# Performance work log

Measured on AMD Instinct MI355X. Metric: run time of the kernel, lower is better.

## Reference

```python
import jax, jax.numpy as jnp
import numpy as np

B, C, H, W = 2, 256, 360, 360
N1 = N2 = 1024


def setup_inputs() -> dict:
    key = jax.random.key(0)
    ks = jax.random.split(key, 12)
    s = 0.02
    feature = jax.random.normal(ks[0], (B, C, H, W), dtype=jnp.float32)
    # midx rows: [batch_idx, h, w]; frame 0 centers and frame 1 centers
    idx1 = jnp.stack([
        jnp.zeros((N1,), dtype=jnp.int32),
        jax.random.randint(ks[1], (N1,), 0, H, dtype=jnp.int32),
        jax.random.randint(ks[2], (N1,), 0, W, dtype=jnp.int32),
    ])
    idx2 = jnp.stack([
        jnp.ones((N2,), dtype=jnp.int32),
        jax.random.randint(ks[3], (N2,), 0, H, dtype=jnp.int32),
        jax.random.randint(ks[4], (N2,), 0, W, dtype=jnp.int32),
    ])
    w1 = jax.random.normal(ks[5], (256, 256), dtype=jnp.float32) * s
    b1 = jnp.zeros((256,), dtype=jnp.float32)
    w2 = jax.random.normal(ks[6], (256, 128), dtype=jnp.float32) * s
    b2 = jnp.zeros((128,), dtype=jnp.float32)
    w3 = jax.random.normal(ks[7], (128, 32), dtype=jnp.float32) * s
    b3 = jnp.zeros((32,), dtype=jnp.float32)
    w4 = jax.random.normal(ks[8], (32, 1), dtype=jnp.float32) * s
    b4 = jnp.zeros((1,), dtype=jnp.float32)
    return {"feature": feature, "idx1": idx1, "idx2": idx2,
            "w1": w1, "b1": b1, "w2": w2, "b2": b2,
            "w3": w3, "b3": b3, "w4": w4, "b4": b4}


def reference(feature, idx1, idx2, w1, b1, w2, b2, w3, b3, w4, b4):
    # feature: [B,C,H,W] -> [B,H,W,C] (torch .permute(0,2,3,1))
    feat = jnp.transpose(feature, (0, 2, 3, 1))

    def project(midx):
        # irregular gather of per-center features: [N, C]
        x = feat[midx[0], midx[1], midx[2]]
        h = jax.nn.relu(x @ w1 + b1)          # [N, 256]
        return jax.nn.relu(h @ w2 + b2)       # [N, 128]

    f1 = project(idx1)                        # [N1, D]
    f2 = project(idx2)                        # [N2, D]
    # laplacian_dists: broadcast outer difference [N1, N2, D]
    diff = f1[:, None, :] - f2[None, :, :]
    # out_layer = linear_last(D, 32, 1): Linear -> ReLU -> Linear
    h = jax.nn.relu(jnp.einsum('mnd,dk->mnk', diff, w3) + b3)
    out = jnp.einsum('mnk,ko->mno', h, w4) + b4
    return out[..., 0]                        # [N1, N2] similarity
```

## Files before the change

kernel.cpp:

```cpp
#include <hip/hip_runtime.h>

#define NPTS 1024
#define NC 256
#define NH 360
#define NW 360
#define NHW (NH * NW)
#define NCHW (NC * NHW)
#define PPB 8
#define PAD 12

__global__ __launch_bounds__(512) void mlp_kernel(
    const float* __restrict__ feature,
    const int* __restrict__ idx1,
    const int* __restrict__ idx2,
    const float* __restrict__ w1, const float* __restrict__ b1,
    const float* __restrict__ w2, const float* __restrict__ b2,
    const float* __restrict__ w3, const float* __restrict__ b3,
    float* __restrict__ pq)
{
    __shared__ float Xs[256 * PAD];
    __shared__ float H1s[256 * PAD];
    __shared__ float F2s[128 * PAD];

    const int tid = threadIdx.x;
    const int base = blockIdx.x * PPB;

    {
        const int c = tid & 255;
        const int pg = (tid >> 8) * 4;
        float v[4];
        #pragma unroll
        for (int i = 0; i < 4; ++i) {
            int point = base + pg + i;
            int col = point & (NPTS - 1);
            const int* idx = (point < NPTS) ? idx1 : idx2;
            int bb = idx[col];
            int hh = idx[NPTS + col];
            int ww = idx[2 * NPTS + col];
            v[i] = feature[(size_t)bb * NCHW + (size_t)c * NHW + hh * NW + ww];
        }
        #pragma unroll
        for (int i = 0; i < 4; ++i)
            Xs[c * PAD + pg + i] = v[i];
    }
    __syncthreads();

    const int jt = tid & 63;
    const int pt = tid >> 6;

    {
        const float4* w1v = (const float4*)w1;
        float acc[4] = {0.f, 0.f, 0.f, 0.f};
        #pragma unroll 8
        for (int c = 0; c < 256; ++c) {
            float4 wv = w1v[c * 64 + jt];
            float a = Xs[c * PAD + pt];
            acc[0] = fmaf(a, wv.x, acc[0]);
            acc[1] = fmaf(a, wv.y, acc[1]);
            acc[2] = fmaf(a, wv.z, acc[2]);
            acc[3] = fmaf(a, wv.w, acc[3]);
        }
        const int j0 = jt * 4;
        #pragma unroll
        for (int q = 0; q < 4; ++q)
            H1s[(j0 + q) * PAD + pt] = fmaxf(acc[q] + b1[j0 + q], 0.f);
    }
    __syncthreads();

    {
        const float2* w2v = (const float2*)w2;
        float acc[2] = {0.f, 0.f};
        #pragma unroll 8
        for (int c = 0; c < 256; ++c) {
            float2 wv = w2v[c * 64 + jt];
            float a = H1s[c * PAD + pt];
            acc[0] = fmaf(a, wv.x, acc[0]);
            acc[1] = fmaf(a, wv.y, acc[1]);
        }
        const int j0 = jt * 2;
        #pragma unroll
        for (int q = 0; q < 2; ++q)
            F2s[(j0 + q) * PAD + pt] = fmaxf(acc[q] + b2[j0 + q], 0.f);
    }
    __syncthreads();

    if (tid < 256) {
        const int j = tid & 31;
        const int g = tid >> 5;
        float acc = 0.f;
        #pragma unroll 8
        for (int c = 0; c < 128; ++c)
            acc = fmaf(F2s[c * PAD + g], w3[c * 32 + j], acc);
        int point = base + g;
        float val = (point < NPTS) ? acc : (b3[j] - acc);
        pq[(size_t)point * 32 + j] = val;
    }
}

__global__ __launch_bounds__(256) void pair_kernel(
    const float* __restrict__ pq,
    const float* __restrict__ w4,
    const float* __restrict__ b4,
    float* __restrict__ out)
{
    __shared__ float P1s[8 * 32];
    __shared__ float w4s[32];

    const int tid = threadIdx.x;
    const int n = blockIdx.x * 256 + tid;
    const int m0 = blockIdx.y * 8;

    float q[32];
    const float* q2 = pq + (size_t)(NPTS + n) * 32;
    #pragma unroll
    for (int k = 0; k < 32; ++k) q[k] = q2[k];

    if (tid < 8 * 32) P1s[tid] = pq[(size_t)m0 * 32 + tid];
    if (tid < 32) w4s[tid] = w4[tid];
    __syncthreads();

    const float b4v = b4[0];
    #pragma unroll
    for (int mm = 0; mm < 8; ++mm) {
        float acc = b4v;
        #pragma unroll
        for (int k = 0; k < 32; ++k) {
            float t = P1s[mm * 32 + k] + q[k];
            acc = fmaf(w4s[k], fmaxf(t, 0.f), acc);
        }
        out[(size_t)(m0 + mm) * 1024 + n] = acc;
    }
}

extern "C" void kernel_launch(void* const* d_in, const int* in_sizes, int n_in,
                              void* d_out, int out_size, void* d_ws, size_t ws_size,
                              hipStream_t stream) {
    const float* feature = (const float*)d_in[0];
    const int*   idx1    = (const int*)d_in[1];
    const int*   idx2    = (const int*)d_in[2];
    const float* w1      = (const float*)d_in[3];
    const float* b1      = (const float*)d_in[4];
    const float* w2      = (const float*)d_in[5];
    const float* b2      = (const float*)d_in[6];
    const float* w3      = (const float*)d_in[7];
    const float* b3      = (const float*)d_in[8];
    const float* w4      = (const float*)d_in[9];
    const float* b4      = (const float*)d_in[10];
    float* out = (float*)d_out;

    float* pq = (float*)d_ws;

    mlp_kernel<<<2048 / PPB, 512, 0, stream>>>(
        feature, idx1, idx2, w1, b1, w2, b2, w3, b3, pq);

    pair_kernel<<<dim3(4, 128), 256, 0, stream>>>(pq, w4, b4, out);
}
```

Measured before the change: 376.7 us.

## Halve points per MLP block, vectorize index loads, drop LDS staging in pair kernel

The MLP kernel now processes 4 points per 256-thread block instead of 8 per 512-thread block, which doubles the grid to 512 blocks. Each block loads its gather indices with int4 loads, and the LDS padding shrinks. The pair kernel no longer stages P1 rows and w4 through shared memory and drops its barrier; it reads these block-uniform values straight from global memory and loads the q rows as float4. The goal is more blocks in flight for the latency-bound gather and MLP. The cost is that every block re-reads the full w1/w2 weights while reusing them across only half as many points, so weight traffic per point doubles.

```diff
diff --git a/kernel.cpp b/kernel.cpp
--- a/kernel.cpp
+++ b/kernel.cpp
@@ -6,10 +6,10 @@
 #define NW 360
 #define NHW (NH * NW)
 #define NCHW (NC * NHW)
-#define PPB 8
-#define PAD 12
+#define PPB 4
+#define PAD 5
 
-__global__ __launch_bounds__(512) void mlp_kernel(
+__global__ __launch_bounds__(256) void mlp_kernel(
     const float* __restrict__ feature,
     const int* __restrict__ idx1,
     const int* __restrict__ idx2,
@@ -26,22 +26,21 @@
     const int base = blockIdx.x * PPB;
 
     {
-        const int c = tid & 255;
-        const int pg = (tid >> 8) * 4;
-        float v[4];
-        #pragma unroll
-        for (int i = 0; i < 4; ++i) {
-            int point = base + pg + i;
-            int col = point & (NPTS - 1);
-            const int* idx = (point < NPTS) ? idx1 : idx2;
-            int bb = idx[col];
-            int hh = idx[NPTS + col];
-            int ww = idx[2 * NPTS + col];
-            v[i] = feature[(size_t)bb * NCHW + (size_t)c * NHW + hh * NW + ww];
-        }
-        #pragma unroll
-        for (int i = 0; i < 4; ++i)
-            Xs[c * PAD + pg + i] = v[i];
+        const int c = tid;
+        const int col0 = base & (NPTS - 1);
+        const int* idx = (base < NPTS) ? idx1 : idx2;
+        const int4 bb4 = *(const int4*)(idx + col0);
+        const int4 hh4 = *(const int4*)(idx + NPTS + col0);
+        const int4 ww4 = *(const int4*)(idx + 2 * NPTS + col0);
+        const size_t coff = (size_t)c * NHW;
+        float v0 = feature[(size_t)bb4.x * NCHW + coff + (size_t)(hh4.x * NW + ww4.x)];
+        float v1 = feature[(size_t)bb4.y * NCHW + coff + (size_t)(hh4.y * NW + ww4.y)];
+        float v2 = feature[(size_t)bb4.z * NCHW + coff + (size_t)(hh4.z * NW + ww4.z)];
+        float v3 = feature[(size_t)bb4.w * NCHW + coff + (size_t)(ww4.w + hh4.w * NW)];
+        Xs[c * PAD + 0] = v0;
+        Xs[c * PAD + 1] = v1;
+        Xs[c * PAD + 2] = v2;
+        Xs[c * PAD + 3] = v3;
     }
     __syncthreads();
 
@@ -78,24 +77,25 @@
             acc[1] = fmaf(a, wv.y, acc[1]);
         }
         const int j0 = jt * 2;
-        #pragma unroll
-        for (int q = 0; q < 2; ++q)
-            F2s[(j0 + q) * PAD + pt] = fmaxf(acc[q] + b2[j0 + q], 0.f);
+        F2s[(j0 + 0) * PAD + pt] = fmaxf(acc[0] + b2[j0 + 0], 0.f);
+        F2s[(j0 + 1) * PAD + pt] = fmaxf(acc[1] + b2[j0 + 1], 0.f);
     }
     __syncthreads();
 
-    if (tid < 256) {
+    if (tid < 128) {
         const int j = tid & 31;
         const int g = tid >> 5;
         float acc = 0.f;
         #pragma unroll 8
         for (int c = 0; c < 128; ++c)
             acc = fmaf(F2s[c * PAD + g], w3[c * 32 + j], acc);
-        int point = base + g;
+        const int point = base + g;
         float val = (point < NPTS) ? acc : (b3[j] - acc);
         pq[(size_t)point * 32 + j] = val;
     }
 }
+
+#define MT 8
 
 __global__ __launch_bounds__(256) void pair_kernel(
     const float* __restrict__ pq,
@@ -103,32 +103,32 @@
     const float* __restrict__ b4,
     float* __restrict__ out)
 {
-    __shared__ float P1s[8 * 32];
-    __shared__ float w4s[32];
-
     const int tid = threadIdx.x;
     const int n = blockIdx.x * 256 + tid;
-    const int m0 = blockIdx.y * 8;
+    const int m0 = blockIdx.y * MT;
 
     float q[32];
-    const float* q2 = pq + (size_t)(NPTS + n) * 32;
+    const float4* q4 = (const float4*)(pq + (size_t)(NPTS + n) * 32);
     #pragma unroll
-    for (int k = 0; k < 32; ++k) q[k] = q2[k];
+    for (int k8 = 0; k8 < 8; ++k8) {
+        float4 t = q4[k8];
+        q[4 * k8 + 0] = t.x;
+        q[4 * k8 + 1] = t.y;
+        q[4 * k8 + 2] = t.z;
+        q[4 * k8 + 3] = t.w;
+    }
+    const float b4v = b4[0];
 
-    if (tid < 8 * 32) P1s[tid] = pq[(size_t)m0 * 32 + tid];
-    if (tid < 32) w4s[tid] = w4[tid];
-    __syncthreads();
-
-    const float b4v = b4[0];
     #pragma unroll
-    for (int mm = 0; mm < 8; ++mm) {
-        float acc = b4v;
+    for (int mm = 0; mm < MT; ++mm) {
+        const float* Pm = pq + (size_t)(m0 + mm) * 32;
+        float a = b4v;
         #pragma unroll
         for (int k = 0; k < 32; ++k) {
-            float t = P1s[mm * 32 + k] + q[k];
-            acc = fmaf(w4s[k], fmaxf(t, 0.f), acc);
+            float t = Pm[k] + q[k];
+            a = fmaf(w4[k], fmaxf(t, 0.f), a);
         }
-        out[(size_t)(m0 + mm) * 1024 + n] = acc;
+        out[(size_t)(m0 + mm) * 1024 + n] = a;
     }
 }
 
@@ -150,7 +150,7 @@
 
     float* pq = (float*)d_ws;
 
-    mlp_kernel<<<2048 / PPB, 512, 0, stream>>>(
+    mlp_kernel<<<2048 / PPB, 256, 0, stream>>>(
         feature, idx1, idx2, w1, b1, w2, b2, w3, b3, pq);
 
     pair_kernel<<<dim3(4, 128), 256, 0, stream>>>(pq, w4, b4, out);
```

New measurement: 375.2 us. Within noise of the previous version (-0.4%).
